# Optimization experiments

Measured on AMD Instinct MI355X. Metric: run time of the kernel, lower is better.

## Reference

```python
import jax, jax.numpy as jnp
import numpy as np

N_NODES = 100000
N_EDGES = 3200000
N_GRAPHS = 1024
F_IN = 4
H = 16


def setup_inputs() -> dict:
    key = jax.random.key(0)
    ks = jax.random.split(key, 12)
    x = jax.random.normal(ks[0], (N_NODES, F_IN), dtype=jnp.float32)
    edge_index = jax.random.randint(ks[1], (2, N_EDGES), 0, N_NODES, dtype=jnp.int64)
    y = jax.random.normal(ks[2], (N_GRAPHS, F_IN), dtype=jnp.float32)
    batch = jnp.sort(jax.random.randint(ks[3], (N_NODES,), 0, N_GRAPHS, dtype=jnp.int64))

    def lin(k, fi, fo):
        s = 1.0 / np.sqrt(fi)
        kw, kb = jax.random.split(k)
        W = jax.random.uniform(kw, (fi, fo), jnp.float32, -s, s)
        b = jax.random.uniform(kb, (fo,), jnp.float32, -s, s)
        return W, b

    W1, b1 = lin(ks[4], F_IN, H)
    W2, b2 = lin(ks[5], H, H)
    W3, b3 = lin(ks[6], H, H)
    fcW1, fcb1 = lin(ks[7], H + 4, H)
    fcW2, fcb2 = lin(ks[8], H, H)
    fcW3, fcb3 = lin(ks[9], H, 1)
    return dict(x=x, edge_index=edge_index, y=y, batch=batch,
                W1=W1, b1=b1, W2=W2, b2=b2, W3=W3, b3=b3,
                fcW1=fcW1, fcb1=fcb1, fcW2=fcW2, fcb2=fcb2, fcW3=fcW3, fcb3=fcb3)


def _gcn_norm(edge_index, n):
    # add self-loops, symmetric normalization (PyG GCNConv default)
    loop = jnp.arange(n, dtype=edge_index.dtype)
    src = jnp.concatenate([edge_index[0], loop])
    dst = jnp.concatenate([edge_index[1], loop])
    deg = jax.ops.segment_sum(jnp.ones_like(dst, dtype=jnp.float32), dst, num_segments=n)
    dinv = jnp.where(deg > 0, jax.lax.rsqrt(deg), 0.0)
    norm = dinv[src] * dinv[dst]  # [E + N]
    return src, dst, norm


def _gcn_conv(x, W, b, src, dst, norm, n):
    h = x @ W                       # [N, out]
    msg = h[src] * norm[:, None]    # gather + scale
    out = jax.ops.segment_sum(msg, dst, num_segments=n)  # scatter-add
    return out + b


def reference(x, edge_index, y, batch, W1, b1, W2, b2, W3, b3,
              fcW1, fcb1, fcW2, fcb2, fcW3, fcb3):
    n = x.shape[0]
    src, dst, norm = _gcn_norm(edge_index, n)
    h = jax.nn.relu(_gcn_conv(x, W1, b1, src, dst, norm, n))
    h = jax.nn.relu(_gcn_conv(h, W2, b2, src, dst, norm, n))
    h = jax.nn.relu(_gcn_conv(h, W3, b3, src, dst, norm, n))
    g = jax.ops.segment_sum(h, batch, num_segments=N_GRAPHS)  # global_add_pool
    g = jnp.concatenate([g, y], axis=1)                       # [G, H+4]
    g = jax.nn.relu(g @ fcW1 + fcb1)
    g = jax.nn.relu(g @ fcW2 + fcb2)
    return g @ fcW3 + fcb3  # [G, 1]
```

## Files before the change

### kernel.cpp

```cpp
#include <hip/hip_runtime.h>
#include <hip/hip_fp16.h>

#define N_NODES 100000
#define N_EDGES 3200000
#define N_GRAPHS 1024
#define F_IN 4
#define H 16

#define NB 256
#define NPB 391
#define CAP 13312
#define CHUNK 4096
#define NBLK ((N_EDGES + CHUNK - 1) / CHUNK)
#define BEPT (CHUNK / 512)
#define EPT_C ((CAP + 1023) / 1024)


__global__ void k_zero_f(float* __restrict__ p, int n) {
    int i = blockIdx.x * blockDim.x + threadIdx.x;
    if (i < n) p[i] = 0.0f;
}


__global__ __launch_bounds__(512) void k_count(const int* __restrict__ dst,
                                               int* __restrict__ blkCnt, int e) {
    __shared__ int h[NB];
    int t = threadIdx.x;
    for (int q = t; q < NB; q += 512) h[q] = 0;
    __syncthreads();
    int e0 = blockIdx.x * CHUNK;
    int e1 = min(e0 + CHUNK, e);
    for (int i = e0 + t; i < e1; i += 512)
        atomicAdd(&h[dst[i] / NPB], 1);
    __syncthreads();
    for (int q = t; q < NB; q += 512) blkCnt[blockIdx.x * NB + q] = h[q];
}

__global__ __launch_bounds__(1024) void k_colscan(const int* __restrict__ blkCnt,
                                                  int* __restrict__ blkBase,
                                                  int* __restrict__ bucketCnt) {
    __shared__ int sc[1024];
    int b = blockIdx.x;
    int t = threadIdx.x;
    int v = (t < NBLK) ? blkCnt[t * NB + b] : 0;
    sc[t] = v;
    __syncthreads();
    for (int off = 1; off < 1024; off <<= 1) {
        int x = (t >= off) ? sc[t - off] : 0;
        __syncthreads();
        sc[t] += x;
        __syncthreads();
    }
    if (t < NBLK) blkBase[t * NB + b] = sc[t] - v;
    if (t == NBLK - 1) bucketCnt[b] = sc[t];
}

__global__ void k_scan_buckets(const int* __restrict__ bucketCnt,
                               int* __restrict__ bucketBase) {
    __shared__ int sh[NB];
    int t = threadIdx.x;
    int v = bucketCnt[t];
    sh[t] = v;
    __syncthreads();
    for (int off = 1; off < NB; off <<= 1) {
        int x = (t >= off) ? sh[t - off] : 0;
        __syncthreads();
        sh[t] += x;
        __syncthreads();
    }
    bucketBase[t] = sh[t] - v;
}

__global__ __launch_bounds__(512) void k_place(const int* __restrict__ src,
                                               const int* __restrict__ dst,
                                               const int* __restrict__ bucketBase,
                                               const int* __restrict__ blkBase,
                                               int* __restrict__ ebuf, int e) {
    __shared__ int cnt[NB];
    __shared__ int st[NB];
    __shared__ int lbase[NB];
    __shared__ int sc[NB];
    __shared__ int lsort[CHUNK];
    __shared__ unsigned short bof[CHUNK];
    int t = threadIdx.x;
    for (int q = t; q < NB; q += 512) {
        cnt[q] = 0;
        lbase[q] = bucketBase[q] + blkBase[blockIdx.x * NB + q];
    }
    __syncthreads();
    int e0 = blockIdx.x * CHUNK;
    int e1 = min(e0 + CHUNK, e);
    int m = e1 - e0;
    int vq[BEPT], bq[BEPT], rq[BEPT];
#pragma unroll
    for (int q = 0; q < BEPT; ++q) {
        int i = e0 + t + q * 512;
        bq[q] = -1;
        if (i < e) {
            int s = src[i];
            int d = dst[i];
            int b = d / NPB;
            int l = d - b * NPB;
            vq[q] = s | (l << 20);
            bq[q] = b;
            rq[q] = atomicAdd(&cnt[b], 1);
        }
    }
    __syncthreads();
    if (t < NB) sc[t] = cnt[t];
    __syncthreads();
    for (int off = 1; off < NB; off <<= 1) {
        int x = (t < NB && t >= off) ? sc[t - off] : 0;
        __syncthreads();
        if (t < NB) sc[t] += x;
        __syncthreads();
    }
    if (t < NB) st[t] = sc[t] - cnt[t];
    __syncthreads();
#pragma unroll
    for (int q = 0; q < BEPT; ++q) {
        if (bq[q] >= 0) {
            int pos = st[bq[q]] + rq[q];
            lsort[pos] = vq[q];
            bof[pos] = (unsigned short)bq[q];
        }
    }
    __syncthreads();
    for (int i = t; i < m; i += 512) {
        int b2 = bof[i];
        ebuf[lbase[b2] + i - st[b2]] = lsort[i];
    }
}

__global__ __launch_bounds__(1024) void k_csrify(const int* __restrict__ ebuf,
                                                 const int* __restrict__ bucketBase,
                                                 const int* __restrict__ bucketCnt,
                                                 const float* __restrict__ x,
                                                 int* __restrict__ csr,
                                                 int* __restrict__ cursor,
                                                 float* __restrict__ dinv,
                                                 __half* __restrict__ ts0) {
    __shared__ int cnt[NPB];
    __shared__ int st[NPB];
    __shared__ int cnt2[NPB];
    __shared__ float sdv[NPB];
    __shared__ int sc[1024];
    __shared__ int lcsr[CAP];
    int t = threadIdx.x;
    int b = blockIdx.x;
    int base = bucketBase[b];
    int m = bucketCnt[b];
    int nbase = b * NPB;
    for (int q = t; q < NPB; q += 1024) { cnt[q] = 0; cnt2[q] = 0; }
    __syncthreads();

    bool fast = (m <= CAP);
    int vq[EPT_C], rq[EPT_C];
    if (fast) {
#pragma unroll
        for (int c = 0; c < EPT_C; ++c) {
            int idx = t + c * 1024;
            vq[c] = -1;
            if (idx < m) {
                int v = ebuf[base + idx];
                vq[c] = v;
                rq[c] = atomicAdd(&cnt[v >> 20], 1);
            }
        }
    } else {
        for (int i = t; i < m; i += 1024)
            atomicAdd(&cnt[ebuf[base + i] >> 20], 1);
    }
    __syncthreads();
    int v0 = (t < NPB) ? cnt[t] : 0;
    sc[t] = v0;
    __syncthreads();
    for (int off = 1; off < 1024; off <<= 1) {
        int xv = (t >= off) ? sc[t - off] : 0;
        __syncthreads();
        sc[t] += xv;
        __syncthreads();
    }
    if (t < NPB) st[t] = sc[t] - v0;
    __syncthreads();
    if (t < NPB) {
        int node = nbase + t;
        if (node < N_NODES) {
            float dv = rsqrtf((float)cnt[t] + 1.0f);
            sdv[t] = dv;
            dinv[node] = dv;
            cursor[node] = base + st[t] + cnt[t];
        }
    }
    __syncthreads();
    for (int idx = t; idx < NPB * F_IN; idx += 1024) {
        int q = idx >> 2;
        int node = nbase + q;
        if (node < N_NODES)
            ts0[node * F_IN + (idx & 3)] =
                __float2half(sdv[q] * x[node * F_IN + (idx & 3)]);
    }
    if (fast) {
#pragma unroll
        for (int c = 0; c < EPT_C; ++c) {
            int v = vq[c];
            if (v >= 0) lcsr[st[v >> 20] + rq[c]] = v & 0xFFFFF;
        }
        __syncthreads();
        for (int i = t; i < m; i += 1024) csr[base + i] = lcsr[i];
    } else {
        for (int i = t; i < m; i += 1024) {
            int v = ebuf[base + i];
            int l = v >> 20;
            int r = atomicAdd(&cnt2[l], 1);
            csr[base + st[l] + r] = v & 0xFFFFF;
        }
    }
}

template <int F, int WAYS>
__global__ void k_gather(const __half* __restrict__ ts, const float* __restrict__ dinv,
                         const int* __restrict__ csr, const int* __restrict__ cursor,
                         float* __restrict__ agg, int n) {
    const int FP = F / 2;
    const int L = FP * WAYS;
    int i = blockIdx.x * (256 / L) + threadIdx.x / L;
    int g = threadIdx.x % L;
    int k2 = g % FP;
    int w = g / FP;
    if (i >= n) return;
    int start = (i == 0) ? 0 : cursor[i - 1];
    int end = cursor[i];
    float ax0 = 0.f, ay0 = 0.f, ax1 = 0.f, ay1 = 0.f;
    int j = start + w;
    for (; j + 3 * WAYS < end; j += 4 * WAYS) {
        int s0 = csr[j];
        int s1 = csr[j + WAYS];
        int s2 = csr[j + 2 * WAYS];
        int s3 = csr[j + 3 * WAYS];
        float2 f0 = __half22float2(*(const __half2*)&ts[s0 * F + 2 * k2]);
        float2 f1 = __half22float2(*(const __half2*)&ts[s1 * F + 2 * k2]);
        float2 f2 = __half22float2(*(const __half2*)&ts[s2 * F + 2 * k2]);
        float2 f3 = __half22float2(*(const __half2*)&ts[s3 * F + 2 * k2]);
        ax0 += f0.x + f2.x; ay0 += f0.y + f2.y;
        ax1 += f1.x + f3.x; ay1 += f1.y + f3.y;
    }
    for (; j < end; j += WAYS) {
        float2 f = __half22float2(*(const __half2*)&ts[csr[j] * F + 2 * k2]);
        ax0 += f.x; ay0 += f.y;
    }
    float sx = ax0 + ax1;
    float sy = ay0 + ay1;
    if (w == 0) {
        float2 f = __half22float2(*(const __half2*)&ts[i * F + 2 * k2]);
        sx += f.x; sy += f.y;
    }
#pragma unroll
    for (int msk = FP; msk < L; msk <<= 1) {
        sx += __shfl_xor(sx, msk, 64);
        sy += __shfl_xor(sy, msk, 64);
    }
    if (w == 0) {
        float dv = dinv[i];
        *(float2*)&agg[i * F + 2 * k2] = make_float2(dv * sx, dv * sy);
    }
}

template <int FI, bool POOL>
__global__ void k_transform(const float* __restrict__ agg, const float* __restrict__ W,
                            const float* __restrict__ bias, const float* __restrict__ dinv,
                            __half* __restrict__ ts_out, const int* __restrict__ batch,
                            float* __restrict__ g, int n) {
    __shared__ float sW[FI * H];
    for (int t = threadIdx.x; t < FI * H; t += blockDim.x) sW[t] = W[t];
    __syncthreads();
    int i = blockIdx.x * 16 + (threadIdx.x >> 4);
    int k = threadIdx.x & 15;
    if (i >= n) return;
    float acc = bias[k];
#pragma unroll
    for (int j = 0; j < FI; j++) acc = fmaf(agg[i * FI + j], sW[j * H + k], acc);
    float h = fmaxf(acc, 0.0f);
    if (POOL) {
        atomicAdd(&g[batch[i] * H + k], h);
    } else {
        ts_out[i * H + k] = __float2half(dinv[i] * h);
    }
}


__global__ void k_mlp(const float* __restrict__ g, const float* __restrict__ y,
                      const float* __restrict__ fcW1, const float* __restrict__ fcb1,
                      const float* __restrict__ fcW2, const float* __restrict__ fcb2,
                      const float* __restrict__ fcW3, const float* __restrict__ fcb3,
                      float* __restrict__ out, int ngraph) {
    int i = blockIdx.x * blockDim.x + threadIdx.x;
    if (i >= ngraph) return;
    float in[H + 4];
#pragma unroll
    for (int k = 0; k < H; k++) in[k] = g[i * H + k];
#pragma unroll
    for (int k = 0; k < 4; k++) in[H + k] = y[i * 4 + k];
    float z1[H];
#pragma unroll
    for (int o = 0; o < H; o++) {
        float a = fcb1[o];
#pragma unroll
        for (int j = 0; j < H + 4; j++) a += in[j] * fcW1[j * H + o];
        z1[o] = fmaxf(a, 0.0f);
    }
    float z2[H];
#pragma unroll
    for (int o = 0; o < H; o++) {
        float a = fcb2[o];
#pragma unroll
        for (int j = 0; j < H; j++) a += z1[j] * fcW2[j * H + o];
        z2[o] = fmaxf(a, 0.0f);
    }
    float a = fcb3[0];
#pragma unroll
    for (int j = 0; j < H; j++) a += z2[j] * fcW3[j];
    out[i] = a;
}


extern "C" void kernel_launch(void* const* d_in, const int* in_sizes, int n_in,
                              void* d_out, int out_size, void* d_ws, size_t ws_size,
                              hipStream_t stream) {
    const float* x    = (const float*)d_in[0];
    const int*   ei   = (const int*)d_in[1];
    const float* y    = (const float*)d_in[2];
    const int*   bat  = (const int*)d_in[3];
    const float* W1   = (const float*)d_in[4];
    const float* b1   = (const float*)d_in[5];
    const float* W2   = (const float*)d_in[6];
    const float* b2   = (const float*)d_in[7];
    const float* W3   = (const float*)d_in[8];
    const float* b3   = (const float*)d_in[9];
    const float* fcW1 = (const float*)d_in[10];
    const float* fcb1 = (const float*)d_in[11];
    const float* fcW2 = (const float*)d_in[12];
    const float* fcb2 = (const float*)d_in[13];
    const float* fcW3 = (const float*)d_in[14];
    const float* fcb3 = (const float*)d_in[15];
    float* out = (float*)d_out;

    const int* src = ei;
    const int* dst = ei + N_EDGES;

    const int B = 256;
    const int GH = N_GRAPHS * H;
    const int gNode16 = (N_NODES + 15) / 16;
    const int gG4  = (N_NODES + 15) / 16;
    const int gG16 = (N_NODES + 7) / 8;

    char* w = (char*)d_ws;
    size_t off = 0;
    int*    bucketCnt    = (int*)(w + off);    off += (size_t)NB * 4;
    int*    bucketBase   = (int*)(w + off);    off += (size_t)NB * 4;
    int*    blkCnt       = (int*)(w + off);    off += (size_t)NBLK * NB * 4;
    int*    blkBase      = (int*)(w + off);    off += (size_t)NBLK * NB * 4;
    int*    cursor       = (int*)(w + off);    off += (size_t)N_NODES * 4;
    float*  dinv         = (float*)(w + off);  off += (size_t)N_NODES * 4;
    int*    ebuf         = (int*)(w + off);    off += (size_t)N_EDGES * 4;
    int*    csr          = (int*)(w + off);    off += (size_t)N_EDGES * 4;
    __half* ts0          = (__half*)(w + off); off += (size_t)N_NODES * F_IN * 2;
    __half* ts1          = (__half*)(w + off); off += (size_t)N_NODES * H * 2;
    __half* ts2          = (__half*)(w + off); off += (size_t)N_NODES * H * 2;
    float*  agg          = (float*)(w + off);  off += (size_t)N_NODES * H * 4;
    float*  g            = (float*)(w + off);  off += (size_t)GH * 4;
    (void)ws_size;

    k_count<<<NBLK, 512, 0, stream>>>(dst, blkCnt, N_EDGES);
    k_colscan<<<NB, 1024, 0, stream>>>(blkCnt, blkBase, bucketCnt);
    k_scan_buckets<<<1, NB, 0, stream>>>(bucketCnt, bucketBase);
    k_place<<<NBLK, 512, 0, stream>>>(src, dst, bucketBase, blkBase, ebuf, N_EDGES);
    k_csrify<<<NB, 1024, 0, stream>>>(ebuf, bucketBase, bucketCnt, x, csr, cursor,
                                      dinv, ts0);

    k_gather<F_IN, 8><<<gG4, B, 0, stream>>>(ts0, dinv, csr, cursor, agg, N_NODES);
    k_transform<F_IN, false><<<gNode16, B, 0, stream>>>(agg, W1, b1, dinv, ts1,
                                                        nullptr, nullptr, N_NODES);
    k_gather<H, 4><<<gG16, B, 0, stream>>>(ts1, dinv, csr, cursor, agg, N_NODES);
    k_transform<H, false><<<gNode16, B, 0, stream>>>(agg, W2, b2, dinv, ts2,
                                                     nullptr, nullptr, N_NODES);
    k_gather<H, 4><<<gG16, B, 0, stream>>>(ts2, dinv, csr, cursor, agg, N_NODES);
    k_zero_f<<<(GH + B - 1) / B, B, 0, stream>>>(g, GH);
    k_transform<H, true><<<gNode16, B, 0, stream>>>(agg, W3, b3, dinv, nullptr,
                                                    bat, g, N_NODES);

    k_mlp<<<(N_GRAPHS + B - 1) / B, B, 0, stream>>>(g, y, fcW1, fcb1, fcW2, fcb2,
                                                    fcW3, fcb3, out, N_GRAPHS);
}
```

Before: 196.8 us.

## Use wave-shuffle scans and add 8-byte-load 16-wide gather kernel

Replaces the shared-memory Hillis-Steele scans in colscan, bucket scan, place and csrify with a wave-level shuffle scan plus a small per-wave offset table, which cuts the number of block barriers. The generic gather loses its 4-way unroll and keeps a 2-way unroll. A new gather kernel for the 16-feature layers has each lane load 4 halves with one 8-byte load, using 8 edge lanes and 4 feature lanes per node. The risks are less memory-level parallelism from the smaller unroll and a different thread-to-node mapping, which assumes gG16 still gives 8 nodes per 256-thread block.

```diff
diff --git a/kernel.cpp b/kernel.cpp
--- a/kernel.cpp
+++ b/kernel.cpp
@@ -16,6 +16,18 @@
 #define EPT_C ((CAP + 1023) / 1024)
 
 
+__device__ __forceinline__ int lane_id() { return threadIdx.x & 63; }
+
+__device__ __forceinline__ int wave_incl_scan(int v) {
+#pragma unroll
+    for (int d = 1; d < 64; d <<= 1) {
+        int x = __shfl_up(v, d, 64);
+        if (lane_id() >= d) v += x;
+    }
+    return v;
+}
+
+
 __global__ void k_zero_f(float* __restrict__ p, int n) {
     int i = blockIdx.x * blockDim.x + threadIdx.x;
     if (i < n) p[i] = 0.0f;
@@ -39,36 +51,41 @@
 __global__ __launch_bounds__(1024) void k_colscan(const int* __restrict__ blkCnt,
                                                   int* __restrict__ blkBase,
                                                   int* __restrict__ bucketCnt) {
-    __shared__ int sc[1024];
+    __shared__ int ws[16];
+    __shared__ int wb[16];
     int b = blockIdx.x;
     int t = threadIdx.x;
     int v = (t < NBLK) ? blkCnt[t * NB + b] : 0;
-    sc[t] = v;
-    __syncthreads();
-    for (int off = 1; off < 1024; off <<= 1) {
-        int x = (t >= off) ? sc[t - off] : 0;
-        __syncthreads();
-        sc[t] += x;
-        __syncthreads();
-    }
-    if (t < NBLK) blkBase[t * NB + b] = sc[t] - v;
-    if (t == NBLK - 1) bucketCnt[b] = sc[t];
+    int incl = wave_incl_scan(v);
+    if (lane_id() == 63) ws[t >> 6] = incl;
+    __syncthreads();
+    if (t == 0) {
+        int acc = 0;
+#pragma unroll
+        for (int q = 0; q < 16; ++q) { wb[q] = acc; acc += ws[q]; }
+    }
+    __syncthreads();
+    int excl = incl - v + wb[t >> 6];
+    if (t < NBLK) blkBase[t * NB + b] = excl;
+    if (t == NBLK - 1) bucketCnt[b] = excl + v;
 }
 
 __global__ void k_scan_buckets(const int* __restrict__ bucketCnt,
                                int* __restrict__ bucketBase) {
-    __shared__ int sh[NB];
+    __shared__ int ws[4];
+    __shared__ int wb[4];
     int t = threadIdx.x;
     int v = bucketCnt[t];
-    sh[t] = v;
-    __syncthreads();
-    for (int off = 1; off < NB; off <<= 1) {
-        int x = (t >= off) ? sh[t - off] : 0;
-        __syncthreads();
-        sh[t] += x;
-        __syncthreads();
-    }
-    bucketBase[t] = sh[t] - v;
+    int incl = wave_incl_scan(v);
+    if (lane_id() == 63) ws[t >> 6] = incl;
+    __syncthreads();
+    if (t == 0) {
+        int acc = 0;
+#pragma unroll
+        for (int q = 0; q < 4; ++q) { wb[q] = acc; acc += ws[q]; }
+    }
+    __syncthreads();
+    bucketBase[t] = incl - v + wb[t >> 6];
 }
 
 __global__ __launch_bounds__(512) void k_place(const int* __restrict__ src,
@@ -79,7 +96,8 @@
     __shared__ int cnt[NB];
     __shared__ int st[NB];
     __shared__ int lbase[NB];
-    __shared__ int sc[NB];
+    __shared__ int ws[4];
+    __shared__ int wb[4];
     __shared__ int lsort[CHUNK];
     __shared__ unsigned short bof[CHUNK];
     int t = threadIdx.x;
@@ -107,15 +125,17 @@
         }
     }
     __syncthreads();
-    if (t < NB) sc[t] = cnt[t];
-    __syncthreads();
-    for (int off = 1; off < NB; off <<= 1) {
-        int x = (t < NB && t >= off) ? sc[t - off] : 0;
-        __syncthreads();
-        if (t < NB) sc[t] += x;
-        __syncthreads();
-    }
-    if (t < NB) st[t] = sc[t] - cnt[t];
+    int v = (t < NB) ? cnt[t] : 0;
+    int incl = wave_incl_scan(v);
+    if (t < NB && lane_id() == 63) ws[t >> 6] = incl;
+    __syncthreads();
+    if (t == 0) {
+        int acc = 0;
+#pragma unroll
+        for (int q = 0; q < 4; ++q) { wb[q] = acc; acc += ws[q]; }
+    }
+    __syncthreads();
+    if (t < NB) st[t] = incl - v + wb[t >> 6];
     __syncthreads();
 #pragma unroll
     for (int q = 0; q < BEPT; ++q) {
@@ -144,7 +164,8 @@
     __shared__ int st[NPB];
     __shared__ int cnt2[NPB];
     __shared__ float sdv[NPB];
-    __shared__ int sc[1024];
+    __shared__ int ws[8];
+    __shared__ int wb[8];
     __shared__ int lcsr[CAP];
     int t = threadIdx.x;
     int b = blockIdx.x;
@@ -173,23 +194,24 @@
     }
     __syncthreads();
     int v0 = (t < NPB) ? cnt[t] : 0;
-    sc[t] = v0;
-    __syncthreads();
-    for (int off = 1; off < 1024; off <<= 1) {
-        int xv = (t >= off) ? sc[t - off] : 0;
-        __syncthreads();
-        sc[t] += xv;
-        __syncthreads();
-    }
-    if (t < NPB) st[t] = sc[t] - v0;
+    int incl = wave_incl_scan(v0);
+    if (t < 448 && lane_id() == 63) ws[t >> 6] = incl;
+    __syncthreads();
+    if (t == 0) {
+        int acc = 0;
+#pragma unroll
+        for (int q = 0; q < 7; ++q) { wb[q] = acc; acc += ws[q]; }
+    }
     __syncthreads();
     if (t < NPB) {
+        int s = incl - v0 + wb[t >> 6];
+        st[t] = s;
         int node = nbase + t;
         if (node < N_NODES) {
             float dv = rsqrtf((float)cnt[t] + 1.0f);
             sdv[t] = dv;
             dinv[node] = dv;
-            cursor[node] = base + st[t] + cnt[t];
+            cursor[node] = base + s + cnt[t];
         }
     }
     __syncthreads();
@@ -233,17 +255,13 @@
     int end = cursor[i];
     float ax0 = 0.f, ay0 = 0.f, ax1 = 0.f, ay1 = 0.f;
     int j = start + w;
-    for (; j + 3 * WAYS < end; j += 4 * WAYS) {
+    for (; j + WAYS < end; j += 2 * WAYS) {
         int s0 = csr[j];
         int s1 = csr[j + WAYS];
-        int s2 = csr[j + 2 * WAYS];
-        int s3 = csr[j + 3 * WAYS];
         float2 f0 = __half22float2(*(const __half2*)&ts[s0 * F + 2 * k2]);
         float2 f1 = __half22float2(*(const __half2*)&ts[s1 * F + 2 * k2]);
-        float2 f2 = __half22float2(*(const __half2*)&ts[s2 * F + 2 * k2]);
-        float2 f3 = __half22float2(*(const __half2*)&ts[s3 * F + 2 * k2]);
-        ax0 += f0.x + f2.x; ay0 += f0.y + f2.y;
-        ax1 += f1.x + f3.x; ay1 += f1.y + f3.y;
+        ax0 += f0.x; ay0 += f0.y;
+        ax1 += f1.x; ay1 += f1.y;
     }
     for (; j < end; j += WAYS) {
         float2 f = __half22float2(*(const __half2*)&ts[csr[j] * F + 2 * k2]);
@@ -263,6 +281,62 @@
     if (w == 0) {
         float dv = dinv[i];
         *(float2*)&agg[i * F + 2 * k2] = make_float2(dv * sx, dv * sy);
+    }
+}
+
+union h4u { float2 f2; __half2 h2[2]; };
+
+__global__ void k_gather16(const __half* __restrict__ ts, const float* __restrict__ dinv,
+                           const int* __restrict__ csr, const int* __restrict__ cursor,
+                           float* __restrict__ agg, int n) {
+    int i = blockIdx.x * 8 + threadIdx.x / 32;
+    int g = threadIdx.x & 31;
+    int k4 = g & 3;
+    int w = g >> 2;
+    if (i >= n) return;
+    int start = (i == 0) ? 0 : cursor[i - 1];
+    int end = cursor[i];
+    float ax0 = 0.f, ay0 = 0.f, az0 = 0.f, aw0 = 0.f;
+    float ax1 = 0.f, ay1 = 0.f, az1 = 0.f, aw1 = 0.f;
+    int j = start + w;
+    for (; j + 8 < end; j += 16) {
+        int s0 = csr[j];
+        int s1 = csr[j + 8];
+        h4u u0, u1;
+        u0.f2 = *(const float2*)&ts[s0 * H + 4 * k4];
+        u1.f2 = *(const float2*)&ts[s1 * H + 4 * k4];
+        float2 l0 = __half22float2(u0.h2[0]);
+        float2 h0 = __half22float2(u0.h2[1]);
+        float2 l1 = __half22float2(u1.h2[0]);
+        float2 h1 = __half22float2(u1.h2[1]);
+        ax0 += l0.x; ay0 += l0.y; az0 += h0.x; aw0 += h0.y;
+        ax1 += l1.x; ay1 += l1.y; az1 += h1.x; aw1 += h1.y;
+    }
+    for (; j < end; j += 8) {
+        h4u u;
+        u.f2 = *(const float2*)&ts[csr[j] * H + 4 * k4];
+        float2 l = __half22float2(u.h2[0]);
+        float2 h = __half22float2(u.h2[1]);
+        ax0 += l.x; ay0 += l.y; az0 += h.x; aw0 += h.y;
+    }
+    float sx = ax0 + ax1, sy = ay0 + ay1, sz = az0 + az1, sw = aw0 + aw1;
+    if (w == 0) {
+        h4u u;
+        u.f2 = *(const float2*)&ts[i * H + 4 * k4];
+        float2 l = __half22float2(u.h2[0]);
+        float2 h = __half22float2(u.h2[1]);
+        sx += l.x; sy += l.y; sz += h.x; sw += h.y;
+    }
+#pragma unroll
+    for (int msk = 4; msk < 32; msk <<= 1) {
+        sx += __shfl_xor(sx, msk, 64);
+        sy += __shfl_xor(sy, msk, 64);
+        sz += __shfl_xor(sz, msk, 64);
+        sw += __shfl_xor(sw, msk, 64);
+    }
+    if (w == 0) {
+        float dv = dinv[i];
+        *(float4*)&agg[i * H + 4 * k4] = make_float4(dv * sx, dv * sy, dv * sz, dv * sw);
     }
 }
 
@@ -381,10 +455,10 @@
     k_gather<F_IN, 8><<<gG4, B, 0, stream>>>(ts0, dinv, csr, cursor, agg, N_NODES);
     k_transform<F_IN, false><<<gNode16, B, 0, stream>>>(agg, W1, b1, dinv, ts1,
                                                         nullptr, nullptr, N_NODES);
-    k_gather<H, 4><<<gG16, B, 0, stream>>>(ts1, dinv, csr, cursor, agg, N_NODES);
+    k_gather16<<<gG16, B, 0, stream>>>(ts1, dinv, csr, cursor, agg, N_NODES);
     k_transform<H, false><<<gNode16, B, 0, stream>>>(agg, W2, b2, dinv, ts2,
                                                      nullptr, nullptr, N_NODES);
-    k_gather<H, 4><<<gG16, B, 0, stream>>>(ts2, dinv, csr, cursor, agg, N_NODES);
+    k_gather16<<<gG16, B, 0, stream>>>(ts2, dinv, csr, cursor, agg, N_NODES);
     k_zero_f<<<(GH + B - 1) / B, B, 0, stream>>>(g, GH);
     k_transform<H, true><<<gNode16, B, 0, stream>>>(agg, W3, b3, dinv, nullptr,
                                                     bat, g, N_NODES);
```

After: 187.7 us. 4.7% less time.
